# Performance work log

Measured on AMD Instinct MI355X. Metric: run time of the kernel, lower is better.

The kernel has to match this reference:

```python
import jax, jax.numpy as jnp
import numpy as np

B, N_IN, N_H, N_OUT = 128, 256, 256, 256


def _bimul(W, X):
    # MatrixBiMul: bilinear map W X W^T, W: [out, in], X: [b, in, in] -> [b, out, out]
    return jnp.einsum('oi,bij,qj->boq', W, X, W)


def setup_inputs() -> dict:
    key = jax.random.key(0)
    ks = jax.random.split(key, 12)
    s_in = 1.0 / np.sqrt(N_IN)
    s_h = 1.0 / np.sqrt(N_H)
    return {
        'input': jax.random.normal(ks[0], (B, N_IN, N_IN), jnp.float32),
        'hidden': jax.random.normal(ks[1], (B, N_H, N_H), jnp.float32),
        'cell': jax.random.normal(ks[2], (B, N_H, N_H), jnp.float32),
        'W_fx': jax.random.normal(ks[3], (N_H, N_IN), jnp.float32) * s_in,
        'W_ix': jax.random.normal(ks[4], (N_H, N_IN), jnp.float32) * s_in,
        'W_ox': jax.random.normal(ks[5], (N_OUT, N_IN), jnp.float32) * s_in,
        'W_gx': jax.random.normal(ks[6], (N_H, N_IN), jnp.float32) * s_in,
        'W_fh': jax.random.normal(ks[7], (N_H, N_H), jnp.float32) * s_h,
        'W_ih': jax.random.normal(ks[8], (N_H, N_H), jnp.float32) * s_h,
        'W_oh': jax.random.normal(ks[9], (N_OUT, N_H), jnp.float32) * s_h,
        'W_gh': jax.random.normal(ks[10], (N_H, N_H), jnp.float32) * s_h,
        'W_oc': jax.random.normal(ks[11], (N_OUT, N_H), jnp.float32) * s_h,
    }


def reference(input, hidden, cell, W_fx, W_ix, W_ox, W_gx, W_fh, W_ih, W_oh, W_gh, W_oc):
    fgate = jax.nn.relu(_bimul(W_fx, input) + _bimul(W_fh, hidden))
    igate = jax.nn.relu(_bimul(W_ix, input) + _bimul(W_ih, hidden))
    ogate = jax.nn.relu(_bimul(W_ox, input) + _bimul(W_oh, hidden))
    ggate = jax.nn.relu(_bimul(W_gx, input) + _bimul(W_gh, hidden))
    c = fgate + cell + igate + ggate  # note: additive, as in source (not fgate*cell)
    h = ogate + jax.nn.relu(_bimul(W_oc, c))
    return (h, c)
```

## Files before the change

### kernel.cpp

```cpp
#include <hip/hip_runtime.h>

typedef __bf16 bf16x8 __attribute__((ext_vector_type(8)));
typedef float f32x4 __attribute__((ext_vector_type(4)));

__device__ __forceinline__ unsigned short f2bf(float f) {
    unsigned int u = __builtin_bit_cast(unsigned int, f);
    u += 0x7fff + ((u >> 16) & 1);
    return (unsigned short)(u >> 16);
}

__device__ __forceinline__ void stage_tile(
    const unsigned short* __restrict__ Ap, int lda,
    const unsigned short* __restrict__ Bp, int ldb,
    unsigned short* lds, int k0, int tid)
{
#pragma unroll
    for (int it = 0; it < 4; ++it) {
        int li = it * 256 + tid;
        int row = li >> 3;
        int sc = ((li & 7) ^ (row & 7)) * 8;
        __builtin_amdgcn_global_load_lds(
            (const __attribute__((address_space(1))) void*)(Ap + (long)row * lda + k0 + sc),
            (__attribute__((address_space(3))) void*)&lds[li * 8], 16, 0, 0);
        __builtin_amdgcn_global_load_lds(
            (const __attribute__((address_space(1))) void*)(Bp + (long)row * ldb + k0 + sc),
            (__attribute__((address_space(3))) void*)&lds[8192 + li * 8], 16, 0, 0);
    }
}

__device__ __forceinline__ void compute_tile(
    const unsigned short* lds, int lane, int wm, int wn, f32x4 (&acc)[4][4])
{
#pragma unroll
    for (int kk = 0; kk < 2; ++kk) {
        const int cl = kk * 4 + (lane >> 4);
        bf16x8 af[4], bfr[4];
#pragma unroll
        for (int m = 0; m < 4; ++m) {
            int row = wm + m * 16 + (lane & 15);
            af[m] = *(const bf16x8*)&lds[row * 64 + ((cl ^ (row & 7)) * 8)];
        }
#pragma unroll
        for (int n = 0; n < 4; ++n) {
            int row = wn + n * 16 + (lane & 15);
            bfr[n] = *(const bf16x8*)&lds[8192 + row * 64 + ((cl ^ (row & 7)) * 8)];
        }
#pragma unroll
        for (int m = 0; m < 4; ++m)
#pragma unroll
            for (int n = 0; n < 4; ++n)
                acc[m][n] = __builtin_amdgcn_mfma_f32_16x16x32_bf16(af[m], bfr[n], acc[m][n], 0, 0, 0);
    }
}

__global__ __launch_bounds__(256)
void cvt_weights(const float* __restrict__ fx, const float* __restrict__ ix,
                 const float* __restrict__ ox, const float* __restrict__ gx,
                 const float* __restrict__ fh, const float* __restrict__ ih,
                 const float* __restrict__ oh, const float* __restrict__ gh,
                 const float* __restrict__ oc,
                 unsigned short* __restrict__ Wcat, unsigned short* __restrict__ Wocb)
{
    int idx = blockIdx.x * 256 + threadIdx.x;
    if (idx < 524288) {
        int g = idx >> 17;
        int rem = idx & 131071;
        int q = rem >> 9;
        int j = rem & 511;
        const float* xs = (g == 0) ? fx : (g == 1) ? ix : (g == 2) ? ox : gx;
        const float* hs = (g == 0) ? fh : (g == 1) ? ih : (g == 2) ? oh : gh;
        float v = (j < 256) ? xs[q * 256 + j] : hs[q * 256 + (j - 256)];
        Wcat[idx] = f2bf(v);
    } else if (idx < 589824) {
        int k = idx - 524288;
        Wocb[k] = f2bf(oc[k]);
    }
}

template <int MODE>
__global__ __launch_bounds__(256)
void gemm_stage1(const float* __restrict__ Xf, const float* __restrict__ Hf,
                 const unsigned short* __restrict__ Wb,
                 unsigned short* __restrict__ Tout)
{
    __shared__ alignas(16) unsigned short lds[17408];

    const int tid = threadIdx.x;
    const int lane = tid & 63;
    const int w = tid >> 6;

    int d = blockIdx.x + 4 * blockIdx.y + 512 * blockIdx.z;
    int swz = (MODE == 0) ? ((d & 7) * 512 + (d >> 3))
                          : ((d & 7) * 64 + (d >> 3));
    const int x = swz & 3;
    const int b = (swz >> 2) & 127;
    const int gz = (MODE == 0) ? (swz >> 9) : 0;
    const int g = gz >> 1, hf = gz & 1;
    const int ti = (x & 1) * 128;
    const int tq = (x >> 1) * 128;
    const int wm = (w >> 1) * 64;
    const int wn = (w & 1) * 64;
    const int ldb = (MODE == 0) ? 512 : 256;

    const float* Ap = ((MODE == 0) ? (hf ? Hf : Xf) : Xf) + (long)b * 65536 + (long)ti * 256;
    const unsigned short* Bp = (MODE == 0)
        ? Wb + (long)g * 131072 + (long)tq * 512 + hf * 256
        : Wb + (long)tq * 256;

    f32x4 acc[4][4];
#pragma unroll
    for (int m = 0; m < 4; ++m)
#pragma unroll
        for (int n = 0; n < 4; ++n)
            acc[m][n] = (f32x4){0.f, 0.f, 0.f, 0.f};

    float4 pre[4][2];
#pragma unroll
    for (int it = 0; it < 4; ++it) {
        int li = it * 256 + tid;
        int row = li >> 3;
        int ck = li & 7;
        const float* ga = Ap + (long)row * 256 + ck * 8;
        pre[it][0] = *(const float4*)ga;
        pre[it][1] = *(const float4*)(ga + 4);
    }

    for (int t = 0; t < 4; ++t) {
        if (t > 0) __syncthreads();
#pragma unroll
        for (int it = 0; it < 4; ++it) {
            int li = it * 256 + tid;
            int row = li >> 3;
            int sc = ((li & 7) ^ (row & 7)) * 8;
            __builtin_amdgcn_global_load_lds(
                (const __attribute__((address_space(1))) void*)(Bp + (long)row * ldb + t * 64 + sc),
                (__attribute__((address_space(3))) void*)&lds[8192 + li * 8], 16, 0, 0);
        }
#pragma unroll
        for (int it = 0; it < 4; ++it) {
            int li = it * 256 + tid;
            int row = li >> 3;
            int ck = li & 7;
            const float* pf = (const float*)&pre[it][0];
            uint4 uv;
            uv.x = (unsigned)f2bf(pf[0]) | ((unsigned)f2bf(pf[1]) << 16);
            uv.y = (unsigned)f2bf(pf[2]) | ((unsigned)f2bf(pf[3]) << 16);
            uv.z = (unsigned)f2bf(pf[4]) | ((unsigned)f2bf(pf[5]) << 16);
            uv.w = (unsigned)f2bf(pf[6]) | ((unsigned)f2bf(pf[7]) << 16);
            *(uint4*)&lds[row * 64 + ((ck ^ (row & 7)) * 8)] = uv;
        }
        __syncthreads();
        if (t < 3) {
#pragma unroll
            for (int it = 0; it < 4; ++it) {
                int li = it * 256 + tid;
                int row = li >> 3;
                int ck = li & 7;
                const float* ga = Ap + (long)row * 256 + (t + 1) * 64 + ck * 8;
                pre[it][0] = *(const float4*)ga;
                pre[it][1] = *(const float4*)(ga + 4);
            }
        }
        compute_tile(lds, lane, wm, wn, acc);
    }

    __syncthreads();
    unsigned short (*ldsT)[136] = (unsigned short(*)[136])lds;
    const int r0 = (lane >> 4) * 4;
    const int c0 = lane & 15;
#pragma unroll
    for (int m = 0; m < 4; ++m)
#pragma unroll
        for (int n = 0; n < 4; ++n)
#pragma unroll
            for (int r = 0; r < 4; ++r) {
                int row = wm + m * 16 + r0 + r;
                int col = wn + n * 16 + c0;
                ldsT[col][row] = f2bf(acc[m][n][r]);
            }
    __syncthreads();
    unsigned short* Cb;
    int ldc;
    if (MODE == 0) { Cb = Tout + (long)g * 16777216 + (long)b * 131072 + hf * 256; ldc = 512; }
    else           { Cb = Tout + (long)b * 65536; ldc = 256; }
#pragma unroll
    for (int it = 0; it < 8; ++it) {
        int idx = it * 256 + tid;
        int qq = idx >> 4;
        int ch = idx & 15;
        uint4 v = *(const uint4*)&ldsT[qq][ch * 8];
        *(uint4*)&Cb[(long)(tq + qq) * ldc + ti + ch * 8] = v;
    }
}

__global__ __launch_bounds__(256)
void gemm_gateB(const unsigned short* __restrict__ Tcat,
                const unsigned short* __restrict__ Wcat,
                const float* __restrict__ cell,
                float* __restrict__ out_c, float* __restrict__ out_h)
{
    __shared__ alignas(16) unsigned short lds[16384];

    const int tid = threadIdx.x;
    const int lane = tid & 63;
    const int w = tid >> 6;
    const int zc = (blockIdx.z == 0);

    int orig = blockIdx.x + 4 * blockIdx.y;
    int swz = (orig & 7) * 64 + (orig >> 3);
    const int x = swz & 3;
    const int b = swz >> 2;
    const int to = (x >> 1) * 128;
    const int tq = (x & 1) * 128;
    const int wm = (w >> 1) * 64;
    const int wn = (w & 1) * 64;

    const int nseg = zc ? 3 : 1;

    f32x4 accc[4][4];
#pragma unroll
    for (int m = 0; m < 4; ++m)
#pragma unroll
        for (int n = 0; n < 4; ++n)
            accc[m][n] = (f32x4){0.f, 0.f, 0.f, 0.f};

    for (int seg = 0; seg < nseg; ++seg) {
        int gv = zc ? (seg + (seg >> 1)) : 2;
        const unsigned short* Ap = Wcat + (long)gv * 131072 + (long)to * 512;
        const unsigned short* Bp = Tcat + (long)gv * 16777216 + (long)b * 131072 + (long)tq * 512;
        f32x4 acc[4][4];
#pragma unroll
        for (int m = 0; m < 4; ++m)
#pragma unroll
            for (int n = 0; n < 4; ++n)
                acc[m][n] = (f32x4){0.f, 0.f, 0.f, 0.f};
        for (int ks = 0; ks < 8; ++ks) {
            if (seg + ks > 0) __syncthreads();
            stage_tile(Ap, 512, Bp, 512, lds, ks * 64, tid);
            __syncthreads();
            compute_tile(lds, lane, wm, wn, acc);
        }
#pragma unroll
        for (int m = 0; m < 4; ++m)
#pragma unroll
            for (int n = 0; n < 4; ++n)
#pragma unroll
                for (int r = 0; r < 4; ++r) {
                    float v = acc[m][n][r];
                    accc[m][n][r] += (v > 0.f ? v : 0.f);
                }
    }

    const int r0 = (lane >> 4) * 4;
    const int c0 = lane & 15;
    if (zc) {
        const float* cb = cell + (long)b * 65536;
        float* co = out_c + (long)b * 65536;
#pragma unroll
        for (int m = 0; m < 4; ++m)
#pragma unroll
            for (int n = 0; n < 4; ++n)
#pragma unroll
                for (int r = 0; r < 4; ++r) {
                    int row = to + wm + m * 16 + r0 + r;
                    int col = tq + wn + n * 16 + c0;
                    co[(long)row * 256 + col] = accc[m][n][r] + cb[(long)row * 256 + col];
                }
    } else {
        float* ho = out_h + (long)b * 65536;
#pragma unroll
        for (int m = 0; m < 4; ++m)
#pragma unroll
            for (int n = 0; n < 4; ++n)
#pragma unroll
                for (int r = 0; r < 4; ++r) {
                    int row = to + wm + m * 16 + r0 + r;
                    int col = tq + wn + n * 16 + c0;
                    ho[(long)row * 256 + col] = accc[m][n][r];
                }
    }
}

__global__ __launch_bounds__(256)
void gemm_hfinal(const unsigned short* __restrict__ Wocb,
                 const unsigned short* __restrict__ ScT,
                 float* __restrict__ out_h)
{
    __shared__ alignas(16) unsigned short lds[16384];

    const int tid = threadIdx.x;
    const int lane = tid & 63;
    const int w = tid >> 6;

    int orig = blockIdx.x + 4 * blockIdx.y;
    int swz = (orig & 7) * 64 + (orig >> 3);
    const int x = swz & 3;
    const int b = swz >> 2;
    const int to = (x >> 1) * 128;
    const int tq = (x & 1) * 128;
    const int wm = (w >> 1) * 64;
    const int wn = (w & 1) * 64;

    const unsigned short* Ap = Wocb + (long)to * 256;
    const unsigned short* Bp = ScT + (long)b * 65536 + (long)tq * 256;

    f32x4 acc[4][4];
#pragma unroll
    for (int m = 0; m < 4; ++m)
#pragma unroll
        for (int n = 0; n < 4; ++n)
            acc[m][n] = (f32x4){0.f, 0.f, 0.f, 0.f};

    for (int t = 0; t < 4; ++t) {
        if (t > 0) __syncthreads();
        stage_tile(Ap, 256, Bp, 256, lds, t * 64, tid);
        __syncthreads();
        compute_tile(lds, lane, wm, wn, acc);
    }

    float* ho = out_h + (long)b * 65536;
    const int r0 = (lane >> 4) * 4;
    const int c0 = lane & 15;
#pragma unroll
    for (int m = 0; m < 4; ++m)
#pragma unroll
        for (int n = 0; n < 4; ++n)
#pragma unroll
            for (int r = 0; r < 4; ++r) {
                int row = to + wm + m * 16 + r0 + r;
                int col = tq + wn + n * 16 + c0;
                float v = acc[m][n][r];
                ho[(long)row * 256 + col] += (v > 0.f ? v : 0.f);
            }
}

extern "C" void kernel_launch(void* const* d_in, const int* in_sizes, int n_in,
                              void* d_out, int out_size, void* d_ws, size_t ws_size,
                              hipStream_t stream)
{
    (void)in_sizes; (void)n_in; (void)out_size; (void)ws_size;

    const float* X    = (const float*)d_in[0];
    const float* H    = (const float*)d_in[1];
    const float* cell = (const float*)d_in[2];
    const float* Wxp[4] = {(const float*)d_in[3], (const float*)d_in[4],
                           (const float*)d_in[5], (const float*)d_in[6]};
    const float* Whp[4] = {(const float*)d_in[7], (const float*)d_in[8],
                           (const float*)d_in[9], (const float*)d_in[10]};
    const float* Wocf = (const float*)d_in[11];

    float* out_h = (float*)d_out;
    float* out_c = out_h + 8388608;

    unsigned short* ws   = (unsigned short*)d_ws;
    unsigned short* ScT  = ws;
    unsigned short* Wcat = ws + 16777216;
    unsigned short* Wocb = ws + 17301504;
    unsigned short* Tcat = ws + 17367040;

    cvt_weights<<<dim3(2304), 256, 0, stream>>>(Wxp[0], Wxp[1], Wxp[2], Wxp[3],
                                                Whp[0], Whp[1], Whp[2], Whp[3],
                                                Wocf, Wcat, Wocb);
    gemm_stage1<0><<<dim3(4, 128, 8), 256, 0, stream>>>(X, H, Wcat, Tcat);
    gemm_gateB<<<dim3(4, 128, 2), 256, 0, stream>>>(Tcat, Wcat, cell, out_c, out_h);
    gemm_stage1<1><<<dim3(4, 128, 1), 256, 0, stream>>>(out_c, nullptr, Wocb, ScT);
    gemm_hfinal<<<dim3(4, 128), 256, 0, stream>>>(Wocb, ScT, out_h);
}
```

Before: 203.6 us.

## Double-buffer LDS tiles across GEMM kernels and merge gate blocks into one

Each GEMM kernel now uses two LDS buffers so the next K-tile's async global-to-LDS loads are issued before the current tile's MFMA compute, with one barrier per step instead of two. The gate kernel no longer launches two z-slices (one doing f/i/g gates, one doing the o gate). Each block now walks all four gates in a single 32-step pipelined loop ordered f, i, g, o, and writes both c and the pre-final h. This doubles LDS use per block, which may lower occupancy, and halves the gate grid, which gives less parallelism.

```diff
diff --git a/kernel.cpp b/kernel.cpp
--- a/kernel.cpp
+++ b/kernel.cpp
@@ -9,7 +9,7 @@
     return (unsigned short)(u >> 16);
 }
 
-__device__ __forceinline__ void stage_tile(
+__device__ __forceinline__ void stage_pair(
     const unsigned short* __restrict__ Ap, int lda,
     const unsigned short* __restrict__ Bp, int ldb,
     unsigned short* lds, int k0, int tid)
@@ -83,7 +83,7 @@
                  const unsigned short* __restrict__ Wb,
                  unsigned short* __restrict__ Tout)
 {
-    __shared__ alignas(16) unsigned short lds[17408];
+    __shared__ alignas(16) unsigned short lds[32768];
 
     const int tid = threadIdx.x;
     const int lane = tid & 63;
@@ -124,18 +124,19 @@
         pre[it][0] = *(const float4*)ga;
         pre[it][1] = *(const float4*)(ga + 4);
     }
-
+#pragma unroll
+    for (int it = 0; it < 4; ++it) {
+        int li = it * 256 + tid;
+        int row = li >> 3;
+        int sc = ((li & 7) ^ (row & 7)) * 8;
+        __builtin_amdgcn_global_load_lds(
+            (const __attribute__((address_space(1))) void*)(Bp + (long)row * ldb + sc),
+            (__attribute__((address_space(3))) void*)&lds[8192 + li * 8], 16, 0, 0);
+    }
+
+#pragma unroll
     for (int t = 0; t < 4; ++t) {
-        if (t > 0) __syncthreads();
-#pragma unroll
-        for (int it = 0; it < 4; ++it) {
-            int li = it * 256 + tid;
-            int row = li >> 3;
-            int sc = ((li & 7) ^ (row & 7)) * 8;
-            __builtin_amdgcn_global_load_lds(
-                (const __attribute__((address_space(1))) void*)(Bp + (long)row * ldb + t * 64 + sc),
-                (__attribute__((address_space(3))) void*)&lds[8192 + li * 8], 16, 0, 0);
-        }
+        unsigned short* buf = lds + (t & 1) * 16384;
 #pragma unroll
         for (int it = 0; it < 4; ++it) {
             int li = it * 256 + tid;
@@ -147,10 +148,11 @@
             uv.y = (unsigned)f2bf(pf[2]) | ((unsigned)f2bf(pf[3]) << 16);
             uv.z = (unsigned)f2bf(pf[4]) | ((unsigned)f2bf(pf[5]) << 16);
             uv.w = (unsigned)f2bf(pf[6]) | ((unsigned)f2bf(pf[7]) << 16);
-            *(uint4*)&lds[row * 64 + ((ck ^ (row & 7)) * 8)] = uv;
+            *(uint4*)&buf[row * 64 + ((ck ^ (row & 7)) * 8)] = uv;
         }
         __syncthreads();
         if (t < 3) {
+            unsigned short* nbuf = lds + ((t + 1) & 1) * 16384;
 #pragma unroll
             for (int it = 0; it < 4; ++it) {
                 int li = it * 256 + tid;
@@ -160,8 +162,17 @@
                 pre[it][0] = *(const float4*)ga;
                 pre[it][1] = *(const float4*)(ga + 4);
             }
-        }
-        compute_tile(lds, lane, wm, wn, acc);
+#pragma unroll
+            for (int it = 0; it < 4; ++it) {
+                int li = it * 256 + tid;
+                int row = li >> 3;
+                int sc = ((li & 7) ^ (row & 7)) * 8;
+                __builtin_amdgcn_global_load_lds(
+                    (const __attribute__((address_space(1))) void*)(Bp + (long)row * ldb + (t + 1) * 64 + sc),
+                    (__attribute__((address_space(3))) void*)&nbuf[8192 + li * 8], 16, 0, 0);
+            }
+        }
+        compute_tile(buf, lane, wm, wn, acc);
     }
 
     __syncthreads();
@@ -199,12 +210,11 @@
                 const float* __restrict__ cell,
                 float* __restrict__ out_c, float* __restrict__ out_h)
 {
-    __shared__ alignas(16) unsigned short lds[16384];
+    __shared__ alignas(16) unsigned short lds[32768];
 
     const int tid = threadIdx.x;
     const int lane = tid & 63;
     const int w = tid >> 6;
-    const int zc = (blockIdx.z == 0);
 
     int orig = blockIdx.x + 4 * blockIdx.y;
     int swz = (orig & 7) * 64 + (orig >> 3);
@@ -215,70 +225,62 @@
     const int wm = (w >> 1) * 64;
     const int wn = (w & 1) * 64;
 
-    const int nseg = zc ? 3 : 1;
-
-    f32x4 accc[4][4];
-#pragma unroll
-    for (int m = 0; m < 4; ++m)
-#pragma unroll
-        for (int n = 0; n < 4; ++n)
+    f32x4 accc[4][4], acc[4][4];
+#pragma unroll
+    for (int m = 0; m < 4; ++m)
+#pragma unroll
+        for (int n = 0; n < 4; ++n) {
             accc[m][n] = (f32x4){0.f, 0.f, 0.f, 0.f};
-
-    for (int seg = 0; seg < nseg; ++seg) {
-        int gv = zc ? (seg + (seg >> 1)) : 2;
-        const unsigned short* Ap = Wcat + (long)gv * 131072 + (long)to * 512;
-        const unsigned short* Bp = Tcat + (long)gv * 16777216 + (long)b * 131072 + (long)tq * 512;
-        f32x4 acc[4][4];
-#pragma unroll
-        for (int m = 0; m < 4; ++m)
-#pragma unroll
-            for (int n = 0; n < 4; ++n)
-                acc[m][n] = (f32x4){0.f, 0.f, 0.f, 0.f};
-        for (int ks = 0; ks < 8; ++ks) {
-            if (seg + ks > 0) __syncthreads();
-            stage_tile(Ap, 512, Bp, 512, lds, ks * 64, tid);
-            __syncthreads();
-            compute_tile(lds, lane, wm, wn, acc);
-        }
-#pragma unroll
-        for (int m = 0; m < 4; ++m)
-#pragma unroll
-            for (int n = 0; n < 4; ++n)
-#pragma unroll
-                for (int r = 0; r < 4; ++r) {
-                    float v = acc[m][n][r];
-                    accc[m][n][r] += (v > 0.f ? v : 0.f);
-                }
-    }
-
+            acc[m][n] = (f32x4){0.f, 0.f, 0.f, 0.f};
+        }
+
+    {
+        const unsigned short* Ap0 = Wcat + (long)to * 512;
+        const unsigned short* Bp0 = Tcat + (long)b * 131072 + (long)tq * 512;
+        stage_pair(Ap0, 512, Bp0, 512, lds, 0, tid);
+    }
+    for (int u = 0; u < 32; ++u) {
+        __syncthreads();
+        if (u + 1 < 32) {
+            int s = (u + 1) >> 3;
+            int gv = s ^ (s >> 1);
+            const unsigned short* Ap = Wcat + (long)gv * 131072 + (long)to * 512;
+            const unsigned short* Bp = Tcat + (long)gv * 16777216 + (long)b * 131072 + (long)tq * 512;
+            stage_pair(Ap, 512, Bp, 512, lds + ((u + 1) & 1) * 16384, ((u + 1) & 7) * 64, tid);
+        }
+        compute_tile(lds + (u & 1) * 16384, lane, wm, wn, acc);
+        if ((u & 7) == 7 && u != 31) {
+#pragma unroll
+            for (int m = 0; m < 4; ++m)
+#pragma unroll
+                for (int n = 0; n < 4; ++n)
+#pragma unroll
+                    for (int r = 0; r < 4; ++r) {
+                        float v = acc[m][n][r];
+                        accc[m][n][r] += (v > 0.f ? v : 0.f);
+                        acc[m][n][r] = 0.f;
+                    }
+        }
+    }
+
+    const float* cb = cell + (long)b * 65536;
+    float* co = out_c + (long)b * 65536;
+    float* ho = out_h + (long)b * 65536;
     const int r0 = (lane >> 4) * 4;
     const int c0 = lane & 15;
-    if (zc) {
-        const float* cb = cell + (long)b * 65536;
-        float* co = out_c + (long)b * 65536;
-#pragma unroll
-        for (int m = 0; m < 4; ++m)
-#pragma unroll
-            for (int n = 0; n < 4; ++n)
-#pragma unroll
-                for (int r = 0; r < 4; ++r) {
-                    int row = to + wm + m * 16 + r0 + r;
-                    int col = tq + wn + n * 16 + c0;
-                    co[(long)row * 256 + col] = accc[m][n][r] + cb[(long)row * 256 + col];
-                }
-    } else {
-        float* ho = out_h + (long)b * 65536;
-#pragma unroll
-        for (int m = 0; m < 4; ++m)
-#pragma unroll
-            for (int n = 0; n < 4; ++n)
-#pragma unroll
-                for (int r = 0; r < 4; ++r) {
-                    int row = to + wm + m * 16 + r0 + r;
-                    int col = tq + wn + n * 16 + c0;
-                    ho[(long)row * 256 + col] = accc[m][n][r];
-                }
-    }
+#pragma unroll
+    for (int m = 0; m < 4; ++m)
+#pragma unroll
+        for (int n = 0; n < 4; ++n)
+#pragma unroll
+            for (int r = 0; r < 4; ++r) {
+                int row = to + wm + m * 16 + r0 + r;
+                int col = tq + wn + n * 16 + c0;
+                long idx = (long)row * 256 + col;
+                co[idx] = accc[m][n][r] + cb[idx];
+                float v = acc[m][n][r];
+                ho[idx] = (v > 0.f ? v : 0.f);
+            }
 }
 
 __global__ __launch_bounds__(256)
@@ -286,7 +288,7 @@
                  const unsigned short* __restrict__ ScT,
                  float* __restrict__ out_h)
 {
-    __shared__ alignas(16) unsigned short lds[16384];
+    __shared__ alignas(16) unsigned short lds[32768];
 
     const int tid = threadIdx.x;
     const int lane = tid & 63;
@@ -311,11 +313,13 @@
         for (int n = 0; n < 4; ++n)
             acc[m][n] = (f32x4){0.f, 0.f, 0.f, 0.f};
 
+    stage_pair(Ap, 256, Bp, 256, lds, 0, tid);
+#pragma unroll
     for (int t = 0; t < 4; ++t) {
-        if (t > 0) __syncthreads();
-        stage_tile(Ap, 256, Bp, 256, lds, t * 64, tid);
         __syncthreads();
-        compute_tile(lds, lane, wm, wn, acc);
+        if (t + 1 < 4)
+            stage_pair(Ap, 256, Bp, 256, lds + ((t + 1) & 1) * 16384, (t + 1) * 64, tid);
+        compute_tile(lds + (t & 1) * 16384, lane, wm, wn, acc);
     }
 
     float* ho = out_h + (long)b * 65536;
@@ -362,7 +366,7 @@
                                                 Whp[0], Whp[1], Whp[2], Whp[3],
                                                 Wocf, Wcat, Wocb);
     gemm_stage1<0><<<dim3(4, 128, 8), 256, 0, stream>>>(X, H, Wcat, Tcat);
-    gemm_gateB<<<dim3(4, 128, 2), 256, 0, stream>>>(Tcat, Wcat, cell, out_c, out_h);
+    gemm_gateB<<<dim3(4, 128), 256, 0, stream>>>(Tcat, Wcat, cell, out_c, out_h);
     gemm_stage1<1><<<dim3(4, 128, 1), 256, 0, stream>>>(out_c, nullptr, Wocb, ScT);
     gemm_hfinal<<<dim3(4, 128), 256, 0, stream>>>(Wocb, ScT, out_h);
 }
```

Result: no change. 205.1 us (+0.8%).
